# Kernel optimization log

Hardware: AMD Instinct MI355X
Metric: run time of the kernel (lower is better)

## Reference

```python
import jax, jax.numpy as jnp
import numpy as np

B, N, F_IN = 32, 1024, 128
DIM, NUM_HEAD = 16, 8
D = DIM * NUM_HEAD  # 128


def setup_inputs() -> dict:
    key = jax.random.key(0)
    ks = jax.random.split(key, 8)
    atom_query = jax.random.normal(ks[0], (B, N, F_IN), dtype=jnp.float32)
    mask = (jax.random.uniform(ks[1], (B, N, 1)) < 0.9).astype(jnp.float32)
    s = 1.0 / np.sqrt(F_IN)
    Wq = jax.random.normal(ks[2], (F_IN, D), dtype=jnp.float32) * s
    bq = jnp.zeros((D,), dtype=jnp.float32)
    Wk = jax.random.normal(ks[3], (F_IN, D), dtype=jnp.float32) * s
    bk = jnp.zeros((D,), dtype=jnp.float32)
    Wv = jax.random.normal(ks[4], (F_IN, D), dtype=jnp.float32) * s
    bv = jnp.zeros((D,), dtype=jnp.float32)
    return {"atom_query": atom_query, "mask": mask,
            "Wq": Wq, "bq": bq, "Wk": Wk, "bk": bk, "Wv": Wv, "bv": bv}


def reference(atom_query, mask, Wq, bq, Wk, bk, Wv, bv):
    scale = 0.5  # self.scale
    q = atom_query @ Wq + bq            # [B, N, D]
    k = atom_query @ Wk + bk            # [B, N, D]
    v = atom_query @ Wv + bv            # [B, N, D] (v_proj=True)
    dk = jnp.asarray(q.shape[-1], jnp.float32) ** (-scale)
    q = q * dk
    energy = jnp.einsum('bqd,bkd->bqk', q, k)      # [B, N, N]
    energy = mask * energy                          # mask broadcasts over k
    agg = jnp.sum(energy, axis=-1, keepdims=True)   # [B, N, 1]
    agg = mask * agg
    # norm=False branch skipped
    agg = agg + (1.0 - mask) * (-1e9)
    attn = jax.nn.softmax(agg, axis=1)              # softmax over query axis
    context = jnp.sum(mask * (attn * v), axis=1)    # [B, D]
    return attn, context
```

## Files before the change

kernel.cpp:

```cpp
#include <hip/hip_runtime.h>

#define B    32
#define N    1024
#define FIN  128
#define CHN  16
#define ROWS 64
#define GRID (B * CHN)

#define OFF_PASUM 0
#define OFF_P     (B * CHN * FIN)
#define OFF_WPART (OFF_P + B * N)
#define OFF_M     (OFF_WPART + B * CHN * FIN)
#define OFF_L     (OFF_M + B * CHN)
#define OFF_S     (OFF_L + B * CHN)

__global__ __launch_bounds__(256) void k_asum(const float* __restrict__ aq,
                                              float* __restrict__ ws) {
    const int b = blockIdx.x >> 4, ch = blockIdx.x & 15;
    const float4* g4 = (const float4*)aq + ((size_t)b * N + ch * ROWS) * 32;
    float4 acc = make_float4(0.f, 0.f, 0.f, 0.f);
    #pragma unroll
    for (int i = 0; i < 8; ++i) {
        float4 v = g4[i * 256 + threadIdx.x];
        acc.x += v.x; acc.y += v.y; acc.z += v.z; acc.w += v.w;
    }
    __shared__ float4 sh[256];
    sh[threadIdx.x] = acc;
    __syncthreads();
    if (threadIdx.x < 32) {
        float4 r = sh[threadIdx.x];
        #pragma unroll
        for (int g = 1; g < 8; ++g) {
            float4 t = sh[g * 32 + threadIdx.x];
            r.x += t.x; r.y += t.y; r.z += t.z; r.w += t.w;
        }
        float4* outp = (float4*)(ws + OFF_PASUM) + (b * CHN + ch) * 32;
        outp[threadIdx.x] = r;
    }
}

__global__ __launch_bounds__(256) void k_main(
    const float* __restrict__ aq, const float* __restrict__ mask,
    const float* __restrict__ Wq, const float* __restrict__ bq,
    const float* __restrict__ Wk, const float* __restrict__ bk,
    float* __restrict__ ws)
{
    const int b = blockIdx.x >> 4, ch = blockIdx.x & 15;
    const int tid = threadIdx.x, f = tid & 127, h = tid >> 7;

    __shared__ float tile[ROWS * FIN];
    __shared__ float red[256];
    __shared__ float asum_s[FIN], ksum_s[FIN], u_s[FIN], mp_s[ROWS];
    __shared__ float c_sh;

    float4 stage[8];
    const float4* g4 = (const float4*)aq + ((size_t)b * N + ch * ROWS) * 32;
    #pragma unroll
    for (int i = 0; i < 8; ++i) stage[i] = g4[i * 256 + tid];

    {
        float a = 0.f;
        #pragma unroll
        for (int c = 0; c < 8; ++c)
            a += ws[OFF_PASUM + (b * CHN + h * 8 + c) * FIN + f];
        red[tid] = a;
    }
    __syncthreads();
    if (tid < FIN) asum_s[f] = red[f] + red[f + 128];
    __syncthreads();
    {
        float ks = 0.f;
        #pragma unroll 8
        for (int i = 0; i < 64; ++i) {
            int fi = h * 64 + i;
            ks += asum_s[fi] * Wk[fi * FIN + f];
        }
        red[tid] = ks;
    }
    __syncthreads();
    if (tid < FIN) ksum_s[f] = red[f] + red[f + 128] + 1024.f * bk[f];
    __syncthreads();
    {
        float uu = 0.f;
        #pragma unroll 8
        for (int i = 0; i < 64; ++i) {
            int d = h * 64 + i;
            uu += Wq[f * FIN + d] * ksum_s[d];
        }
        red[tid] = uu;
    }
    __syncthreads();
    if (tid < FIN) u_s[f] = red[f] + red[f + 128];
    if (tid < 64) {
        float cc = bq[tid] * ksum_s[tid] + bq[tid + 64] * ksum_s[tid + 64];
        #pragma unroll
        for (int off = 32; off > 0; off >>= 1) cc += __shfl_xor(cc, off);
        if (tid == 0) c_sh = cc;
    }
    {
        float4* t4 = (float4*)tile;
        #pragma unroll
        for (int i = 0; i < 8; ++i) {
            int g = i * 256 + tid;
            int row = g >> 5, c4 = g & 31;
            t4[row * 32 + (c4 ^ (row & 31))] = stage[i];
        }
    }
    __syncthreads();

    {
        const int r = tid & 63, q = tid >> 6;
        const float4* t4 = (const float4*)tile;
        const float4* u4 = (const float4*)u_s;
        float acc = 0.f;
        #pragma unroll
        for (int jj = 0; jj < 8; ++jj) {
            int j = q * 8 + jj;
            float4 a = t4[r * 32 + (j ^ (r & 31))];
            float4 uu = u4[j];
            acc += a.x * uu.x + a.y * uu.y + a.z * uu.z + a.w * uu.w;
        }
        red[tid] = acc;
    }
    __syncthreads();
    if (tid < ROWS) {
        const float dkc = 0.08838834764831845f;
        float dot = red[tid] + red[tid + 64] + red[tid + 128] + red[tid + 192];
        float m = mask[b * N + ch * ROWS + tid];
        float raw = dkc * (dot + c_sh);
        float aggv = m * raw + (1.f - m) * (-1e9f);
        float Mc = aggv;
        #pragma unroll
        for (int off = 32; off > 0; off >>= 1) Mc = fmaxf(Mc, __shfl_xor(Mc, off));
        float p = __expf(aggv - Mc);
        float mp = m * p;
        ws[OFF_P + b * N + ch * ROWS + tid] = p;
        mp_s[tid] = mp;
        float Lc = p, Sc = mp;
        #pragma unroll
        for (int off = 32; off > 0; off >>= 1) {
            Lc += __shfl_xor(Lc, off);
            Sc += __shfl_xor(Sc, off);
        }
        if (tid == 0) {
            ws[OFF_M + b * CHN + ch] = Mc;
            ws[OFF_L + b * CHN + ch] = Lc;
            ws[OFF_S + b * CHN + ch] = Sc;
        }
    }
    __syncthreads();
    {
        float w = 0.f;
        #pragma unroll 8
        for (int i = 0; i < 32; ++i) {
            int r = h * 32 + i;
            w += mp_s[r] * tile[r * FIN + ((((f >> 2) ^ (r & 31)) << 2) | (f & 3))];
        }
        red[tid] = w;
    }
    __syncthreads();
    if (tid < FIN)
        ws[OFF_WPART + (b * CHN + ch) * FIN + f] = red[f] + red[f + 128];
}

__global__ __launch_bounds__(256) void k_final(const float* __restrict__ Wv,
                                               const float* __restrict__ bv,
                                               const float* __restrict__ ws,
                                               float* __restrict__ out) {
    const int b = blockIdx.x >> 2, sub = blockIdx.x & 3;
    const int tid = threadIdx.x, f = tid & 127, h = tid >> 7;
    float M = -3.0e38f;
    #pragma unroll
    for (int c = 0; c < CHN; ++c) M = fmaxf(M, ws[OFF_M + b * CHN + c]);
    float Em[CHN], L = 0.f, S = 0.f;
    #pragma unroll
    for (int c = 0; c < CHN; ++c) {
        float e = __expf(ws[OFF_M + b * CHN + c] - M);
        Em[c] = e;
        L += e * ws[OFF_L + b * CHN + c];
        S += e * ws[OFF_S + b * CHN + c];
    }
    const float invL = 1.f / L;
    {
        int n = sub * 256 + tid;
        out[b * N + n] = ws[OFF_P + b * N + n] * Em[sub * 4 + (tid >> 6)] * invL;
    }
    if (sub != 0) return;
    __shared__ float wsh[FIN];
    __shared__ float red[256];
    {
        float w = 0.f;
        #pragma unroll
        for (int c = 0; c < 8; ++c)
            w += Em[h * 8 + c] * ws[OFF_WPART + (b * CHN + h * 8 + c) * FIN + f];
        red[tid] = w;
    }
    __syncthreads();
    if (tid < FIN) wsh[f] = red[f] + red[f + 128];
    __syncthreads();
    {
        float ctx = 0.f;
        #pragma unroll 8
        for (int i = 0; i < 64; ++i) {
            int fi = h * 64 + i;
            ctx += wsh[fi] * Wv[fi * FIN + f];
        }
        red[tid] = ctx;
    }
    __syncthreads();
    if (tid < FIN)
        out[B * N + b * FIN + f] = (red[f] + red[f + 128]) * invL + S * invL * bv[f];
}

extern "C" void kernel_launch(void* const* d_in, const int* in_sizes, int n_in,
                              void* d_out, int out_size, void* d_ws, size_t ws_size,
                              hipStream_t stream) {
    const float* aq   = (const float*)d_in[0];
    const float* mask = (const float*)d_in[1];
    const float* Wq   = (const float*)d_in[2];
    const float* bq   = (const float*)d_in[3];
    const float* Wk   = (const float*)d_in[4];
    const float* bk   = (const float*)d_in[5];
    const float* Wv   = (const float*)d_in[6];
    const float* bv   = (const float*)d_in[7];
    float* ws  = (float*)d_ws;
    float* out = (float*)d_out;

    k_asum <<<GRID,  256, 0, stream>>>(aq, ws);
    k_main <<<GRID,  256, 0, stream>>>(aq, mask, Wq, bq, Wk, bk, ws);
    k_final<<<B * 4, 256, 0, stream>>>(Wv, bv, ws, out);
}
```

Measured before the change: 101.6 us.

## Fuse three kernels into one cooperative kernel with grid-wide syncs

```diff
diff --git a/kernel.cpp b/kernel.cpp
--- a/kernel.cpp
+++ b/kernel.cpp
@@ -1,4 +1,7 @@
 #include <hip/hip_runtime.h>
+#include <hip/hip_cooperative_groups.h>
+
+namespace cg = cooperative_groups;
 
 #define B    32
 #define N    1024
@@ -14,49 +17,49 @@
 #define OFF_L     (OFF_M + B * CHN)
 #define OFF_S     (OFF_L + B * CHN)
 
-__global__ __launch_bounds__(256) void k_asum(const float* __restrict__ aq,
-                                              float* __restrict__ ws) {
-    const int b = blockIdx.x >> 4, ch = blockIdx.x & 15;
-    const float4* g4 = (const float4*)aq + ((size_t)b * N + ch * ROWS) * 32;
-    float4 acc = make_float4(0.f, 0.f, 0.f, 0.f);
-    #pragma unroll
-    for (int i = 0; i < 8; ++i) {
-        float4 v = g4[i * 256 + threadIdx.x];
-        acc.x += v.x; acc.y += v.y; acc.z += v.z; acc.w += v.w;
-    }
-    __shared__ float4 sh[256];
-    sh[threadIdx.x] = acc;
-    __syncthreads();
-    if (threadIdx.x < 32) {
-        float4 r = sh[threadIdx.x];
-        #pragma unroll
-        for (int g = 1; g < 8; ++g) {
-            float4 t = sh[g * 32 + threadIdx.x];
-            r.x += t.x; r.y += t.y; r.z += t.z; r.w += t.w;
-        }
-        float4* outp = (float4*)(ws + OFF_PASUM) + (b * CHN + ch) * 32;
-        outp[threadIdx.x] = r;
-    }
-}
-
-__global__ __launch_bounds__(256) void k_main(
+__global__ __launch_bounds__(256, 2) void k_fused(
     const float* __restrict__ aq, const float* __restrict__ mask,
     const float* __restrict__ Wq, const float* __restrict__ bq,
     const float* __restrict__ Wk, const float* __restrict__ bk,
-    float* __restrict__ ws)
+    const float* __restrict__ Wv, const float* __restrict__ bv,
+    float* __restrict__ ws, float* __restrict__ out)
 {
-    const int b = blockIdx.x >> 4, ch = blockIdx.x & 15;
+    const int g = blockIdx.x;
+    const int b = g >> 4, ch = g & 15;
     const int tid = threadIdx.x, f = tid & 127, h = tid >> 7;
 
     __shared__ float tile[ROWS * FIN];
-    __shared__ float red[256];
+    __shared__ float4 sh4[256];
+    float* red = (float*)sh4;
     __shared__ float asum_s[FIN], ksum_s[FIN], u_s[FIN], mp_s[ROWS];
     __shared__ float c_sh;
 
-    float4 stage[8];
-    const float4* g4 = (const float4*)aq + ((size_t)b * N + ch * ROWS) * 32;
-    #pragma unroll
-    for (int i = 0; i < 8; ++i) stage[i] = g4[i * 256 + tid];
+    {
+        const float4* g4 = (const float4*)aq + ((size_t)b * N + ch * ROWS) * 32;
+        float4* t4 = (float4*)tile;
+        float4 accv = make_float4(0.f, 0.f, 0.f, 0.f);
+        #pragma unroll
+        for (int i = 0; i < 8; ++i) {
+            float4 v = g4[i * 256 + tid];
+            int gg = i * 256 + tid;
+            int row = gg >> 5, c4 = gg & 31;
+            t4[row * 32 + (c4 ^ (row & 31))] = v;
+            accv.x += v.x; accv.y += v.y; accv.z += v.z; accv.w += v.w;
+        }
+        sh4[tid] = accv;
+        __syncthreads();
+        if (tid < 32) {
+            float4 r = sh4[tid];
+            #pragma unroll
+            for (int gr = 1; gr < 8; ++gr) {
+                float4 t = sh4[gr * 32 + tid];
+                r.x += t.x; r.y += t.y; r.z += t.z; r.w += t.w;
+            }
+            float4* outp = (float4*)(ws + OFF_PASUM) + (b * CHN + ch) * 32;
+            outp[tid] = r;
+        }
+    }
+    cg::this_grid().sync();
 
     {
         float a = 0.f;
@@ -96,15 +99,6 @@
         #pragma unroll
         for (int off = 32; off > 0; off >>= 1) cc += __shfl_xor(cc, off);
         if (tid == 0) c_sh = cc;
-    }
-    {
-        float4* t4 = (float4*)tile;
-        #pragma unroll
-        for (int i = 0; i < 8; ++i) {
-            int g = i * 256 + tid;
-            int row = g >> 5, c4 = g & 31;
-            t4[row * 32 + (c4 ^ (row & 31))] = stage[i];
-        }
     }
     __syncthreads();
 
@@ -161,55 +155,53 @@
     __syncthreads();
     if (tid < FIN)
         ws[OFF_WPART + (b * CHN + ch) * FIN + f] = red[f] + red[f + 128];
-}
-
-__global__ __launch_bounds__(256) void k_final(const float* __restrict__ Wv,
-                                               const float* __restrict__ bv,
-                                               const float* __restrict__ ws,
-                                               float* __restrict__ out) {
-    const int b = blockIdx.x >> 2, sub = blockIdx.x & 3;
-    const int tid = threadIdx.x, f = tid & 127, h = tid >> 7;
-    float M = -3.0e38f;
-    #pragma unroll
-    for (int c = 0; c < CHN; ++c) M = fmaxf(M, ws[OFF_M + b * CHN + c]);
-    float Em[CHN], L = 0.f, S = 0.f;
-    #pragma unroll
-    for (int c = 0; c < CHN; ++c) {
-        float e = __expf(ws[OFF_M + b * CHN + c] - M);
-        Em[c] = e;
-        L += e * ws[OFF_L + b * CHN + c];
-        S += e * ws[OFF_S + b * CHN + c];
-    }
-    const float invL = 1.f / L;
-    {
-        int n = sub * 256 + tid;
-        out[b * N + n] = ws[OFF_P + b * N + n] * Em[sub * 4 + (tid >> 6)] * invL;
-    }
-    if (sub != 0) return;
-    __shared__ float wsh[FIN];
-    __shared__ float red[256];
-    {
-        float w = 0.f;
-        #pragma unroll
-        for (int c = 0; c < 8; ++c)
-            w += Em[h * 8 + c] * ws[OFF_WPART + (b * CHN + h * 8 + c) * FIN + f];
-        red[tid] = w;
-    }
-    __syncthreads();
-    if (tid < FIN) wsh[f] = red[f] + red[f + 128];
-    __syncthreads();
-    {
-        float ctx = 0.f;
-        #pragma unroll 8
-        for (int i = 0; i < 64; ++i) {
-            int fi = h * 64 + i;
-            ctx += wsh[fi] * Wv[fi * FIN + f];
-        }
-        red[tid] = ctx;
-    }
-    __syncthreads();
-    if (tid < FIN)
-        out[B * N + b * FIN + f] = (red[f] + red[f + 128]) * invL + S * invL * bv[f];
+
+    cg::this_grid().sync();
+
+    if (g >= B * 4) return;
+    {
+        const int bb = g >> 2, sub = g & 3;
+        float M = -3.0e38f;
+        #pragma unroll
+        for (int c = 0; c < CHN; ++c) M = fmaxf(M, ws[OFF_M + bb * CHN + c]);
+        float Em[CHN], L = 0.f, S = 0.f;
+        #pragma unroll
+        for (int c = 0; c < CHN; ++c) {
+            float e = __expf(ws[OFF_M + bb * CHN + c] - M);
+            Em[c] = e;
+            L += e * ws[OFF_L + bb * CHN + c];
+            S += e * ws[OFF_S + bb * CHN + c];
+        }
+        const float invL = 1.f / L;
+        {
+            int n = sub * 256 + tid;
+            out[bb * N + n] = ws[OFF_P + bb * N + n] * Em[sub * 4 + (tid >> 6)] * invL;
+        }
+        if (sub != 0) return;
+        float* wsh = u_s;
+        {
+            float w = 0.f;
+            #pragma unroll
+            for (int c = 0; c < 8; ++c)
+                w += Em[h * 8 + c] * ws[OFF_WPART + (bb * CHN + h * 8 + c) * FIN + f];
+            red[tid] = w;
+        }
+        __syncthreads();
+        if (tid < FIN) wsh[f] = red[f] + red[f + 128];
+        __syncthreads();
+        {
+            float ctx = 0.f;
+            #pragma unroll 8
+            for (int i = 0; i < 64; ++i) {
+                int fi = h * 64 + i;
+                ctx += wsh[fi] * Wv[fi * FIN + f];
+            }
+            red[tid] = ctx;
+        }
+        __syncthreads();
+        if (tid < FIN)
+            out[B * N + bb * FIN + f] = (red[f] + red[f + 128]) * invL + S * invL * bv[f];
+    }
 }
 
 extern "C" void kernel_launch(void* const* d_in, const int* in_sizes, int n_in,
@@ -226,7 +218,7 @@
     float* ws  = (float*)d_ws;
     float* out = (float*)d_out;
 
-    k_asum <<<GRID,  256, 0, stream>>>(aq, ws);
-    k_main <<<GRID,  256, 0, stream>>>(aq, mask, Wq, bq, Wk, bk, ws);
-    k_final<<<B * 4, 256, 0, stream>>>(Wv, bv, ws, out);
+    void* args[] = {&aq, &mask, &Wq, &bq, &Wk, &bk, &Wv, &bv, &ws, &out};
+    hipLaunchCooperativeKernel((const void*)k_fused, dim3(GRID), dim3(256),
+                               args, 0, stream);
 }
```

After: 205.3 us. 2.02x slower.

## Move per-chunk Wk/Wq projections into pre-kernel and fuse final reduction via last-block atomic

Applied to the files above, without the earlier changes.

```diff
diff --git a/kernel.cpp b/kernel.cpp
--- a/kernel.cpp
+++ b/kernel.cpp
@@ -7,51 +7,100 @@
 #define ROWS 64
 #define GRID (B * CHN)
 
-#define OFF_PASUM 0
-#define OFF_P     (B * CHN * FIN)
+#define OFF_PU    0
+#define OFF_PC    (B * CHN * FIN)
+#define OFF_P     (OFF_PC + B * CHN)
 #define OFF_WPART (OFF_P + B * N)
 #define OFF_M     (OFF_WPART + B * CHN * FIN)
 #define OFF_L     (OFF_M + B * CHN)
 #define OFF_S     (OFF_L + B * CHN)
-
-__global__ __launch_bounds__(256) void k_asum(const float* __restrict__ aq,
-                                              float* __restrict__ ws) {
+#define OFF_CNT   (OFF_S + B * CHN)
+
+__global__ __launch_bounds__(256) void k_pre(const float* __restrict__ aq,
+                                             const float* __restrict__ Wq,
+                                             const float* __restrict__ bq,
+                                             const float* __restrict__ Wk,
+                                             const float* __restrict__ bk,
+                                             float* __restrict__ ws) {
     const int b = blockIdx.x >> 4, ch = blockIdx.x & 15;
-    const float4* g4 = (const float4*)aq + ((size_t)b * N + ch * ROWS) * 32;
-    float4 acc = make_float4(0.f, 0.f, 0.f, 0.f);
-    #pragma unroll
-    for (int i = 0; i < 8; ++i) {
-        float4 v = g4[i * 256 + threadIdx.x];
-        acc.x += v.x; acc.y += v.y; acc.z += v.z; acc.w += v.w;
-    }
-    __shared__ float4 sh[256];
-    sh[threadIdx.x] = acc;
-    __syncthreads();
-    if (threadIdx.x < 32) {
-        float4 r = sh[threadIdx.x];
-        #pragma unroll
-        for (int g = 1; g < 8; ++g) {
-            float4 t = sh[g * 32 + threadIdx.x];
-            r.x += t.x; r.y += t.y; r.z += t.z; r.w += t.w;
-        }
-        float4* outp = (float4*)(ws + OFF_PASUM) + (b * CHN + ch) * 32;
-        outp[threadIdx.x] = r;
+    const int tid = threadIdx.x, f = tid & 127, h = tid >> 7;
+
+    __shared__ float4 sh4[256];
+    float* red = (float*)sh4;
+    __shared__ float asum_s[FIN], pks_s[FIN];
+
+    if (ch == 0 && tid == 0) ((unsigned int*)ws)[OFF_CNT + b] = 0u;
+
+    {
+        const float4* g4 = (const float4*)aq + ((size_t)b * N + ch * ROWS) * 32;
+        float4 acc = make_float4(0.f, 0.f, 0.f, 0.f);
+        #pragma unroll
+        for (int i = 0; i < 8; ++i) {
+            float4 v = g4[i * 256 + tid];
+            acc.x += v.x; acc.y += v.y; acc.z += v.z; acc.w += v.w;
+        }
+        sh4[tid] = acc;
+        __syncthreads();
+        if (tid < 32) {
+            float4 r = sh4[tid];
+            #pragma unroll
+            for (int gr = 1; gr < 8; ++gr) {
+                float4 t = sh4[gr * 32 + tid];
+                r.x += t.x; r.y += t.y; r.z += t.z; r.w += t.w;
+            }
+            ((float4*)asum_s)[tid] = r;
+        }
+    }
+    __syncthreads();
+    {
+        float ks = 0.f;
+        #pragma unroll 8
+        for (int i = 0; i < 64; ++i) {
+            int fi = h * 64 + i;
+            ks += asum_s[fi] * Wk[fi * FIN + f];
+        }
+        red[tid] = ks;
+    }
+    __syncthreads();
+    if (tid < FIN) {
+        float pk = red[f] + red[f + 128];
+        if (ch == 0) pk += 1024.f * bk[f];
+        pks_s[f] = pk;
+    }
+    __syncthreads();
+    {
+        float uu = 0.f;
+        #pragma unroll 8
+        for (int i = 0; i < 64; ++i) {
+            int d = h * 64 + i;
+            uu += Wq[f * FIN + d] * pks_s[d];
+        }
+        red[tid] = uu;
+    }
+    __syncthreads();
+    if (tid < FIN)
+        ws[OFF_PU + (b * CHN + ch) * FIN + f] = red[f] + red[f + 128];
+    if (tid < 64) {
+        float cc = bq[tid] * pks_s[tid] + bq[tid + 64] * pks_s[tid + 64];
+        #pragma unroll
+        for (int off = 32; off > 0; off >>= 1) cc += __shfl_xor(cc, off);
+        if (tid == 0) ws[OFF_PC + b * CHN + ch] = cc;
     }
 }
 
 __global__ __launch_bounds__(256) void k_main(
     const float* __restrict__ aq, const float* __restrict__ mask,
-    const float* __restrict__ Wq, const float* __restrict__ bq,
-    const float* __restrict__ Wk, const float* __restrict__ bk,
-    float* __restrict__ ws)
+    const float* __restrict__ Wv, const float* __restrict__ bv,
+    float* __restrict__ ws, float* __restrict__ out)
 {
     const int b = blockIdx.x >> 4, ch = blockIdx.x & 15;
     const int tid = threadIdx.x, f = tid & 127, h = tid >> 7;
 
     __shared__ float tile[ROWS * FIN];
     __shared__ float red[256];
-    __shared__ float asum_s[FIN], ksum_s[FIN], u_s[FIN], mp_s[ROWS];
+    __shared__ float u_s[FIN], mp_s[ROWS];
     __shared__ float c_sh;
+    __shared__ int   last_s;
 
     float4 stage[8];
     const float4* g4 = (const float4*)aq + ((size_t)b * N + ch * ROWS) * 32;
@@ -59,42 +108,19 @@
     for (int i = 0; i < 8; ++i) stage[i] = g4[i * 256 + tid];
 
     {
-        float a = 0.f;
+        float uu = 0.f;
         #pragma unroll
         for (int c = 0; c < 8; ++c)
-            a += ws[OFF_PASUM + (b * CHN + h * 8 + c) * FIN + f];
-        red[tid] = a;
-    }
-    __syncthreads();
-    if (tid < FIN) asum_s[f] = red[f] + red[f + 128];
-    __syncthreads();
-    {
-        float ks = 0.f;
-        #pragma unroll 8
-        for (int i = 0; i < 64; ++i) {
-            int fi = h * 64 + i;
-            ks += asum_s[fi] * Wk[fi * FIN + f];
-        }
-        red[tid] = ks;
-    }
-    __syncthreads();
-    if (tid < FIN) ksum_s[f] = red[f] + red[f + 128] + 1024.f * bk[f];
-    __syncthreads();
-    {
-        float uu = 0.f;
-        #pragma unroll 8
-        for (int i = 0; i < 64; ++i) {
-            int d = h * 64 + i;
-            uu += Wq[f * FIN + d] * ksum_s[d];
-        }
+            uu += ws[OFF_PU + (b * CHN + h * 8 + c) * FIN + f];
         red[tid] = uu;
     }
+    float cc = 0.f;
+    if (tid < 16) cc = ws[OFF_PC + b * CHN + tid];
     __syncthreads();
     if (tid < FIN) u_s[f] = red[f] + red[f + 128];
-    if (tid < 64) {
-        float cc = bq[tid] * ksum_s[tid] + bq[tid + 64] * ksum_s[tid + 64];
-        #pragma unroll
-        for (int off = 32; off > 0; off >>= 1) cc += __shfl_xor(cc, off);
+    if (tid < 16) {
+        #pragma unroll
+        for (int off = 8; off > 0; off >>= 1) cc += __shfl_xor(cc, off);
         if (tid == 0) c_sh = cc;
     }
     {
@@ -161,49 +187,52 @@
     __syncthreads();
     if (tid < FIN)
         ws[OFF_WPART + (b * CHN + ch) * FIN + f] = red[f] + red[f + 128];
-}
-
-__global__ __launch_bounds__(256) void k_final(const float* __restrict__ Wv,
-                                               const float* __restrict__ bv,
-                                               const float* __restrict__ ws,
-                                               float* __restrict__ out) {
-    const int b = blockIdx.x >> 2, sub = blockIdx.x & 3;
-    const int tid = threadIdx.x, f = tid & 127, h = tid >> 7;
+
+    __threadfence();
+    __syncthreads();
+    if (tid == 0) {
+        unsigned int old = atomicAdd((unsigned int*)ws + OFF_CNT + b, 1u);
+        last_s = (old == (unsigned)(CHN - 1));
+    }
+    __syncthreads();
+    if (!last_s) return;
+    __threadfence();
+
     float M = -3.0e38f;
     #pragma unroll
     for (int c = 0; c < CHN; ++c) M = fmaxf(M, ws[OFF_M + b * CHN + c]);
-    float Em[CHN], L = 0.f, S = 0.f;
+    float L = 0.f, S = 0.f;
     #pragma unroll
     for (int c = 0; c < CHN; ++c) {
         float e = __expf(ws[OFF_M + b * CHN + c] - M);
-        Em[c] = e;
         L += e * ws[OFF_L + b * CHN + c];
         S += e * ws[OFF_S + b * CHN + c];
     }
     const float invL = 1.f / L;
     {
-        int n = sub * 256 + tid;
-        out[b * N + n] = ws[OFF_P + b * N + n] * Em[sub * 4 + (tid >> 6)] * invL;
-    }
-    if (sub != 0) return;
-    __shared__ float wsh[FIN];
-    __shared__ float red[256];
+        float4 p4 = ((const float4*)(ws + OFF_P + b * N))[tid];
+        float sc = __expf(ws[OFF_M + b * CHN + (tid >> 4)] - M) * invL;
+        float4 o4 = make_float4(p4.x * sc, p4.y * sc, p4.z * sc, p4.w * sc);
+        ((float4*)(out + b * N))[tid] = o4;
+    }
     {
         float w = 0.f;
         #pragma unroll
-        for (int c = 0; c < 8; ++c)
-            w += Em[h * 8 + c] * ws[OFF_WPART + (b * CHN + h * 8 + c) * FIN + f];
+        for (int c = 0; c < 8; ++c) {
+            float e = __expf(ws[OFF_M + b * CHN + h * 8 + c] - M);
+            w += e * ws[OFF_WPART + (b * CHN + h * 8 + c) * FIN + f];
+        }
         red[tid] = w;
     }
     __syncthreads();
-    if (tid < FIN) wsh[f] = red[f] + red[f + 128];
+    if (tid < FIN) u_s[f] = red[f] + red[f + 128];
     __syncthreads();
     {
         float ctx = 0.f;
         #pragma unroll 8
         for (int i = 0; i < 64; ++i) {
             int fi = h * 64 + i;
-            ctx += wsh[fi] * Wv[fi * FIN + f];
+            ctx += u_s[fi] * Wv[fi * FIN + f];
         }
         red[tid] = ctx;
     }
@@ -226,7 +255,6 @@
     float* ws  = (float*)d_ws;
     float* out = (float*)d_out;
 
-    k_asum <<<GRID,  256, 0, stream>>>(aq, ws);
-    k_main <<<GRID,  256, 0, stream>>>(aq, mask, Wq, bq, Wk, bk, ws);
-    k_final<<<B * 4, 256, 0, stream>>>(Wv, bv, ws, out);
+    k_pre <<<GRID, 256, 0, stream>>>(aq, Wq, bq, Wk, bk, ws);
+    k_main<<<GRID, 256, 0, stream>>>(aq, mask, Wv, bv, ws, out);
 }
```

New measurement: 138.9 us. 1.37x slower.
